# Performance work log

Hardware: AMD Instinct MI355X
Metric: run time of the kernel (lower is better)

## Reference

```python
import jax, jax.numpy as jnp
import numpy as np

N = 50000   # nodes
E = 600000  # directed edges (self-loops added inside reference, per GCNConv default)
G = 64      # graphs in the batch
D = 128     # in_features
H = 128     # hidden_channels
C = 10      # num_classes


def setup_inputs() -> dict:
    key = jax.random.key(0)
    ks = jax.random.split(key, 9)
    x = jax.random.normal(ks[0], (N, D), dtype=jnp.float32)
    edge_index = jax.random.randint(ks[1], (2, E), 0, N, dtype=jnp.int64)
    batch = jnp.sort(jax.random.randint(ks[2], (N,), 0, G, dtype=jnp.int64))
    # GCNConv weights (glorot-ish scale) and biases; final linear layer
    W1 = jax.random.normal(ks[3], (D, H), dtype=jnp.float32) / np.sqrt(D).astype(np.float32)
    b1 = jnp.zeros((H,), dtype=jnp.float32)
    W2 = jax.random.normal(ks[4], (H, H), dtype=jnp.float32) / np.sqrt(H).astype(np.float32)
    b2 = jnp.zeros((H,), dtype=jnp.float32)
    Wlin = jax.random.normal(ks[5], (H, C), dtype=jnp.float32) / np.sqrt(H).astype(np.float32)
    blin = jnp.zeros((C,), dtype=jnp.float32)
    return {"x": x, "W1": W1, "b1": b1, "W2": W2, "b2": b2,
            "Wlin": Wlin, "blin": blin, "edge_index": edge_index, "batch": batch}


def _gcn_conv(x, W, b, row, col, norm):
    # x' = D^{-1/2}(A+I)D^{-1/2} (x W) + b ; aggregate messages from row (src) into col (dst)
    h = x @ W                                   # [N, H] dense GEMM
    msg = norm[:, None] * h[row]                # gather by source index [E+N, H]
    out = jax.ops.segment_sum(msg, col, num_segments=N)  # scatter-add to targets
    return out + b


def reference(x, W1, b1, W2, b2, Wlin, blin, edge_index, batch):
    loops = jnp.arange(N, dtype=edge_index.dtype)
    row = jnp.concatenate([edge_index[0], loops])   # sources (+ self loops)
    col = jnp.concatenate([edge_index[1], loops])   # targets (+ self loops)
    # symmetric degree normalization (degrees >= 1 thanks to self loops)
    deg = jax.ops.segment_sum(jnp.ones_like(col, dtype=jnp.float32), col, num_segments=N)
    dinv = jax.lax.rsqrt(deg)
    norm = dinv[row] * dinv[col]                    # [E+N]

    h = jax.nn.relu(_gcn_conv(x, W1, b1, row, col, norm))
    h = _gcn_conv(h, W2, b2, row, col, norm)

    # global mean pool over graphs
    sums = jax.ops.segment_sum(h, batch, num_segments=G)                       # [G, H]
    cnt = jax.ops.segment_sum(jnp.ones((N,), dtype=jnp.float32), batch, num_segments=G)
    pooled = sums / jnp.maximum(cnt, 1.0)[:, None]

    return pooled @ Wlin + blin                     # logits [G, C]
```

## Files before the change

### kernel.cpp

```cpp
#include <hip/hip_runtime.h>

#define NN 50000
#define NE 600000
#define NG 64
#define DIM 128
#define NCLS 10
#define SB 196
#define NNP 50176
#define KBLK 392
#define KCH 128
#define CAP 64
#define E2B ((NE / 2 + 255) / 256)
#define NT32 (NNP / 32)
#define BSW_TAIL_START ((size_t)(NN >> 5) * 4096)

typedef unsigned short ushort;
typedef unsigned char uchar;
typedef __attribute__((ext_vector_type(8))) short short8;
typedef __attribute__((ext_vector_type(4))) float float4v;
typedef __attribute__((ext_vector_type(2))) float float2v;

__device__ __forceinline__ ushort f2bf(float f) {
    unsigned u = __float_as_uint(f);
    u += 0x7fff + ((u >> 16) & 1);
    return (ushort)(u >> 16);
}
__device__ __forceinline__ uchar f2fp8(float f) {
    int p = __builtin_amdgcn_cvt_pk_fp8_f32(f, f, 0, false);
    return (uchar)(p & 0xff);
}
__device__ __forceinline__ void accfp8(float* a, uint2 v) {
    float2v p0 = __builtin_amdgcn_cvt_pk_f32_fp8(v.x, false);
    float2v p1 = __builtin_amdgcn_cvt_pk_f32_fp8(v.x, true);
    float2v p2 = __builtin_amdgcn_cvt_pk_f32_fp8(v.y, false);
    float2v p3 = __builtin_amdgcn_cvt_pk_f32_fp8(v.y, true);
    a[0] += p0[0]; a[1] += p0[1]; a[2] += p1[0]; a[3] += p1[1];
    a[4] += p2[0]; a[5] += p2[1]; a[6] += p3[0]; a[7] += p3[1];
}

__global__ void k_init(int* __restrict__ cnt, const float* __restrict__ W1,
                       ushort* __restrict__ Wsw, float* __restrict__ T,
                       float* __restrict__ dinv, float* __restrict__ P,
                       ushort* __restrict__ Bsw) {
    int b = blockIdx.x, t = threadIdx.x;
    if (b < SB) {
        int i = b * 256 + t;
        if (i < NN) cnt[i] = 0;
    } else if (b < SB + 64) {
        int tid = (b - SB) * 256 + t;
        int j = tid & 7;
        int lane = (tid >> 3) & 63;
        int frag = tid >> 9;
        int nt = frag >> 2, kc = frag & 3;
        int k = kc * 32 + (lane >> 4) * 8 + j;
        int n = nt * 16 + (lane & 15);
        Wsw[tid] = f2bf(W1[k * DIM + n]);
    } else if (b < SB + 64 + 784) {
        float4* w4 = (float4*)T;
        int base = (b - SB - 64) * 256 + t;
#pragma unroll
        for (int i = 0; i < 4; ++i)
            w4[base + i * 200704] = make_float4(0.f, 0.f, 0.f, 0.f);
    } else if (b == SB + 64 + 784) {
        if (t < NNP - NN) dinv[NN + t] = 0.f;
        float4* p4 = (float4*)P;
#pragma unroll
        for (int i = 0; i < 8; ++i)
            p4[i * 256 + t] = make_float4(0.f, 0.f, 0.f, 0.f);
    } else {
        int idx = (b - (SB + 64 + 785)) * 256 + t;
        ((float4*)(Bsw + BSW_TAIL_START))[idx] = make_float4(0.f, 0.f, 0.f, 0.f);
    }
}

__global__ void k_fill(const int* __restrict__ row, const int* __restrict__ col,
                       int* __restrict__ cnt, int* __restrict__ ell) {
    int e = (blockIdx.x * blockDim.x + threadIdx.x) * 2;
    if (e < NE) {
        int2 r = *(const int2*)(row + e);
        int2 c = *(const int2*)(col + e);
        int p0 = atomicAdd(&cnt[c.x], 1);
        if (p0 < CAP) ell[c.x * CAP + p0] = r.x;
        int p1 = atomicAdd(&cnt[c.y], 1);
        if (p1 < CAP) ell[c.y * CAP + p1] = r.y;
    }
}

__global__ __launch_bounds__(256) void k_gemm_mfma(const float* __restrict__ Ain,
                                                   const ushort* __restrict__ Wsw,
                                                   const int* __restrict__ cnt,
                                                   uchar* __restrict__ Hs,
                                                   float* __restrict__ dinv) {
    const int t = threadIdx.x;
    const int wave = t >> 6, lane = t & 63;
    const int m = lane & 15, quad = lane >> 4;
    const int row0 = blockIdx.x * 64 + wave * 16;

    short8 bfrag[8][4];
#pragma unroll
    for (int nt = 0; nt < 8; ++nt)
#pragma unroll
        for (int kc = 0; kc < 4; ++kc)
            bfrag[nt][kc] = *(const short8*)(Wsw + ((nt * 4 + kc) * 64 + lane) * 8);

    float4v acc[8];
#pragma unroll
    for (int nt = 0; nt < 8; ++nt) acc[nt] = (float4v){0.f, 0.f, 0.f, 0.f};

    const int row = row0 + m;
    const int rclamp = row < NN ? row : NN - 1;

#pragma unroll
    for (int kc = 0; kc < 4; ++kc) {
        const float* ap = Ain + (size_t)rclamp * DIM + kc * 32 + quad * 8;
        float4 v0 = *(const float4*)ap;
        float4 v1 = *(const float4*)(ap + 4);
        union { short8 v; ushort u[8]; } tmp;
        tmp.u[0] = f2bf(v0.x); tmp.u[1] = f2bf(v0.y);
        tmp.u[2] = f2bf(v0.z); tmp.u[3] = f2bf(v0.w);
        tmp.u[4] = f2bf(v1.x); tmp.u[5] = f2bf(v1.y);
        tmp.u[6] = f2bf(v1.z); tmp.u[7] = f2bf(v1.w);
        short8 a = tmp.v;
#pragma unroll
        for (int nt = 0; nt < 8; ++nt)
            acc[nt] = __builtin_amdgcn_mfma_f32_16x16x32_bf16(a, bfrag[nt][kc], acc[nt], 0, 0, 0);
    }

#pragma unroll
    for (int reg = 0; reg < 4; ++reg) {
        int r = row0 + quad * 4 + reg;
        if (r < NN) {
            float d = rsqrtf(1.0f + (float)cnt[r]);
            if (m == 0) dinv[r] = d;
#pragma unroll
            for (int nt = 0; nt < 8; ++nt)
                Hs[(size_t)r * DIM + nt * 16 + m] = f2fp8(d * acc[nt][reg]);
        }
    }
}

__global__ __launch_bounds__(256) void k_gather_ell(const int* __restrict__ ell,
                                                    const int* __restrict__ deg,
                                                    const int* __restrict__ batch,
                                                    const float* __restrict__ bias,
                                                    const uchar* __restrict__ Hs,
                                                    float* __restrict__ T,
                                                    ushort* __restrict__ out) {
    int gt = blockIdx.x * blockDim.x + threadIdx.x;
    int node = gt >> 4, lane = gt & 15;
    if (node >= NN) return;
    const int* rowp = ell + node * CAP;
    int end = min(deg[node], CAP);
    const float d = rsqrtf(1.0f + (float)end);
    float* Trow = T + (size_t)batch[node] * NNP;
    const size_t off = (size_t)lane * 8;

    float a[8] = {0.f, 0.f, 0.f, 0.f, 0.f, 0.f, 0.f, 0.f};
    accfp8(a, *(const uint2*)(Hs + (size_t)node * DIM + off));
    if (lane == 0) atomicAdd(&Trow[node], d);

    int e = 0;
    for (; e + 8 <= end; e += 8) {
        int r0 = rowp[e], r1 = rowp[e + 1], r2 = rowp[e + 2], r3 = rowp[e + 3];
        int r4 = rowp[e + 4], r5 = rowp[e + 5], r6 = rowp[e + 6], r7 = rowp[e + 7];
        if (lane < 8) atomicAdd(&Trow[rowp[e + lane]], d);
        uint2 v0 = *(const uint2*)(Hs + (size_t)r0 * DIM + off);
        uint2 v1 = *(const uint2*)(Hs + (size_t)r1 * DIM + off);
        uint2 v2 = *(const uint2*)(Hs + (size_t)r2 * DIM + off);
        uint2 v3 = *(const uint2*)(Hs + (size_t)r3 * DIM + off);
        uint2 v4 = *(const uint2*)(Hs + (size_t)r4 * DIM + off);
        uint2 v5 = *(const uint2*)(Hs + (size_t)r5 * DIM + off);
        uint2 v6 = *(const uint2*)(Hs + (size_t)r6 * DIM + off);
        uint2 v7 = *(const uint2*)(Hs + (size_t)r7 * DIM + off);
        accfp8(a, v0); accfp8(a, v1); accfp8(a, v2); accfp8(a, v3);
        accfp8(a, v4); accfp8(a, v5); accfp8(a, v6); accfp8(a, v7);
    }
    for (; e + 4 <= end; e += 4) {
        int r0 = rowp[e], r1 = rowp[e + 1], r2 = rowp[e + 2], r3 = rowp[e + 3];
        if (lane < 4) atomicAdd(&Trow[rowp[e + lane]], d);
        uint2 v0 = *(const uint2*)(Hs + (size_t)r0 * DIM + off);
        uint2 v1 = *(const uint2*)(Hs + (size_t)r1 * DIM + off);
        uint2 v2 = *(const uint2*)(Hs + (size_t)r2 * DIM + off);
        uint2 v3 = *(const uint2*)(Hs + (size_t)r3 * DIM + off);
        accfp8(a, v0); accfp8(a, v1); accfp8(a, v2); accfp8(a, v3);
    }
    for (; e < end; ++e) {
        int r = rowp[e];
        if (lane == 0) atomicAdd(&Trow[r], d);
        accfp8(a, *(const uint2*)(Hs + (size_t)r * DIM + off));
    }

    float4 b0 = *(const float4*)(bias + off);
    float4 b1 = *(const float4*)(bias + off + 4);
    a[0] = fmaxf(fmaf(a[0], d, b0.x), 0.f); a[1] = fmaxf(fmaf(a[1], d, b0.y), 0.f);
    a[2] = fmaxf(fmaf(a[2], d, b0.z), 0.f); a[3] = fmaxf(fmaf(a[3], d, b0.w), 0.f);
    a[4] = fmaxf(fmaf(a[4], d, b1.x), 0.f); a[5] = fmaxf(fmaf(a[5], d, b1.y), 0.f);
    a[6] = fmaxf(fmaf(a[6], d, b1.z), 0.f); a[7] = fmaxf(fmaf(a[7], d, b1.w), 0.f);

    ushort* bp = out + (size_t)(node >> 5) * 4096 + (size_t)(lane >> 1) * 512
                     + (size_t)((node >> 3) & 3) * 128 + (size_t)(lane & 1) * 64
                     + (size_t)(node & 7);
    bp[0]  = f2bf(a[0]); bp[8]  = f2bf(a[1]); bp[16] = f2bf(a[2]); bp[24] = f2bf(a[3]);
    bp[32] = f2bf(a[4]); bp[40] = f2bf(a[5]); bp[48] = f2bf(a[6]); bp[56] = f2bf(a[7]);
}

__global__ __launch_bounds__(256) void k_pool_gemm(const float* __restrict__ T,
                                                   const float* __restrict__ dinv,
                                                   const ushort* __restrict__ Bsw,
                                                   float* __restrict__ P) {
    const int t = threadIdx.x;
    const int wave = t >> 6, lane = t & 63;
    const int m = lane & 15, quad = lane >> 4;
    const int g = wave * 16 + m;
    const int k0 = blockIdx.x * KCH;

    float4v acc[8];
#pragma unroll
    for (int nt = 0; nt < 8; ++nt) acc[nt] = (float4v){0.f, 0.f, 0.f, 0.f};

#pragma unroll
    for (int s = 0; s < KCH / 32; ++s) {
        const int kb = k0 + s * 32 + quad * 8;
        const float* ap = T + (size_t)g * NNP + kb;
        float4 a0 = *(const float4*)ap;
        float4 a1 = *(const float4*)(ap + 4);
        float4 d0 = *(const float4*)(dinv + kb);
        float4 d1 = *(const float4*)(dinv + kb + 4);
        union { short8 v; ushort u[8]; } af;
        af.u[0] = f2bf(a0.x * d0.x); af.u[1] = f2bf(a0.y * d0.y);
        af.u[2] = f2bf(a0.z * d0.z); af.u[3] = f2bf(a0.w * d0.w);
        af.u[4] = f2bf(a1.x * d1.x); af.u[5] = f2bf(a1.y * d1.y);
        af.u[6] = f2bf(a1.z * d1.z); af.u[7] = f2bf(a1.w * d1.w);

        const int t32 = (k0 >> 5) + s;
        const ushort* bb = Bsw + (size_t)t32 * 4096 + (size_t)lane * 8;
#pragma unroll
        for (int nt = 0; nt < 8; ++nt) {
            short8 bv = *(const short8*)(bb + nt * 512);
            acc[nt] = __builtin_amdgcn_mfma_f32_16x16x32_bf16(af.v, bv, acc[nt], 0, 0, 0);
        }
    }

#pragma unroll
    for (int reg = 0; reg < 4; ++reg) {
        int gg = wave * 16 + quad * 4 + reg;
#pragma unroll
        for (int nt = 0; nt < 8; ++nt)
            atomicAdd(&P[gg * DIM + nt * 16 + m], acc[nt][reg]);
    }
}

__global__ __launch_bounds__(128) void k_final(const float* __restrict__ P,
                                               const float* __restrict__ W2,
                                               const float* __restrict__ b2,
                                               const float* __restrict__ Wlin,
                                               const float* __restrict__ blin,
                                               const int* __restrict__ batch,
                                               float* __restrict__ out) {
    const int g = blockIdx.x;
    const int t = threadIdx.x;
    int start;
    { int a = 0, b = NN; while (a < b) { int m = (a + b) >> 1; if (batch[m] < g) a = m + 1; else b = m; } start = a; }
    int end;
    { int a = 0, b = NN; while (a < b) { int m = (a + b) >> 1; if (batch[m] < g + 1) a = m + 1; else b = m; } end = a; }
    const int cnt = end - start;

    __shared__ float Pl[DIM];
    Pl[t] = P[g * DIM + t];
    __syncthreads();
    float acc = 0.f;
    for (int k = 0; k < DIM; ++k) acc += Pl[k] * W2[k * DIM + t];
    __shared__ float pooled[DIM];
    pooled[t] = (cnt > 0) ? (acc / (float)cnt + b2[t]) : 0.f;
    __syncthreads();
    if (t < NCLS) {
        float s2 = blin[t];
        for (int k = 0; k < DIM; ++k) s2 += pooled[k] * Wlin[k * NCLS + t];
        out[g * NCLS + t] = s2;
    }
}

extern "C" void kernel_launch(void* const* d_in, const int* in_sizes, int n_in,
                              void* d_out, int out_size, void* d_ws, size_t ws_size,
                              hipStream_t stream) {
    const float* x    = (const float*)d_in[0];
    const float* W1   = (const float*)d_in[1];
    const float* b1   = (const float*)d_in[2];
    const float* W2   = (const float*)d_in[3];
    const float* b2   = (const float*)d_in[4];
    const float* Wlin = (const float*)d_in[5];
    const float* blin = (const float*)d_in[6];
    const int* eidx   = (const int*)d_in[7];
    const int* batch  = (const int*)d_in[8];
    float* out = (float*)d_out;

    char* ws = (char*)d_ws;
    int*    cnt   = (int*)(ws + 0);
    float*  dinv  = (float*)(ws + 200000);
    int*    ell   = (int*)(ws + 400704);
    ushort* Wsw   = (ushort*)(ws + 13200704);
    float*  T     = (float*)(ws + 13233472);
    uchar*  Hs1   = (uchar*)(ws + 26078528);
    ushort* Bsw   = (ushort*)(ws + 32478528);
    float*  P     = (float*)(ws + 45323584);

    const int* erow = eidx;
    const int* ecol = eidx + NE;

    k_init<<<SB + 64 + 784 + 1 + 12, 256, 0, stream>>>(cnt, W1, Wsw, T, dinv, P, Bsw);
    k_fill<<<E2B, 256, 0, stream>>>(erow, ecol, cnt, ell);

    const int gemm_grid = (NN + 63) / 64;
    const int node_grid = (NN * 16 + 255) / 256;

    k_gemm_mfma<<<gemm_grid, 256, 0, stream>>>(x, Wsw, cnt, Hs1, dinv);
    k_gather_ell<<<node_grid, 256, 0, stream>>>(ell, cnt, batch, b1, Hs1, T, Bsw);

    k_pool_gemm<<<KBLK, 256, 0, stream>>>(T, dinv, Bsw, P);

    k_final<<<NG, 128, 0, stream>>>(P, W2, b2, Wlin, blin, batch, out);
}
```

Before: 215.2 us.

## Compress ELL indices to u16, coalesce gather output via LDS, replace pool atomics with partials

Stores ELL neighbor indices as 16-bit values and loads them with vector loads, halving index traffic in fill and gather. The gather kernel now transposes its bf16 output through shared memory so the swizzled B-operand buffer is written in coalesced 16-byte stores instead of scattered 2-byte stores. The pooled GEMM writes per-block partial results instead of atomics, and the final kernel reduces the partials with 512 threads. The u16 indices rely on the node count fitting in 16 bits, and the extra barrier and partial buffer add some overhead.

```diff
diff --git a/kernel.cpp b/kernel.cpp
--- a/kernel.cpp
+++ b/kernel.cpp
@@ -11,7 +11,6 @@
 #define KCH 128
 #define CAP 64
 #define E2B ((NE / 2 + 255) / 256)
-#define NT32 (NNP / 32)
 #define BSW_TAIL_START ((size_t)(NN >> 5) * 4096)
 
 typedef unsigned short ushort;
@@ -40,8 +39,7 @@
 
 __global__ void k_init(int* __restrict__ cnt, const float* __restrict__ W1,
                        ushort* __restrict__ Wsw, float* __restrict__ T,
-                       float* __restrict__ dinv, float* __restrict__ P,
-                       ushort* __restrict__ Bsw) {
+                       float* __restrict__ dinv, ushort* __restrict__ Bsw) {
     int b = blockIdx.x, t = threadIdx.x;
     if (b < SB) {
         int i = b * 256 + t;
@@ -63,10 +61,6 @@
             w4[base + i * 200704] = make_float4(0.f, 0.f, 0.f, 0.f);
     } else if (b == SB + 64 + 784) {
         if (t < NNP - NN) dinv[NN + t] = 0.f;
-        float4* p4 = (float4*)P;
-#pragma unroll
-        for (int i = 0; i < 8; ++i)
-            p4[i * 256 + t] = make_float4(0.f, 0.f, 0.f, 0.f);
     } else {
         int idx = (b - (SB + 64 + 785)) * 256 + t;
         ((float4*)(Bsw + BSW_TAIL_START))[idx] = make_float4(0.f, 0.f, 0.f, 0.f);
@@ -74,15 +68,15 @@
 }
 
 __global__ void k_fill(const int* __restrict__ row, const int* __restrict__ col,
-                       int* __restrict__ cnt, int* __restrict__ ell) {
+                       int* __restrict__ cnt, ushort* __restrict__ ell) {
     int e = (blockIdx.x * blockDim.x + threadIdx.x) * 2;
     if (e < NE) {
         int2 r = *(const int2*)(row + e);
         int2 c = *(const int2*)(col + e);
         int p0 = atomicAdd(&cnt[c.x], 1);
-        if (p0 < CAP) ell[c.x * CAP + p0] = r.x;
+        if (p0 < CAP) ell[(size_t)c.x * CAP + p0] = (ushort)r.x;
         int p1 = atomicAdd(&cnt[c.y], 1);
-        if (p1 < CAP) ell[c.y * CAP + p1] = r.y;
+        if (p1 < CAP) ell[(size_t)c.y * CAP + p1] = (ushort)r.y;
     }
 }
 
@@ -139,17 +133,17 @@
     }
 }
 
-__global__ __launch_bounds__(256) void k_gather_ell(const int* __restrict__ ell,
+__global__ __launch_bounds__(256) void k_gather_ell(const ushort* __restrict__ ell,
                                                     const int* __restrict__ deg,
                                                     const int* __restrict__ batch,
                                                     const float* __restrict__ bias,
                                                     const uchar* __restrict__ Hs,
                                                     float* __restrict__ T,
-                                                    ushort* __restrict__ out) {
-    int gt = blockIdx.x * blockDim.x + threadIdx.x;
-    int node = gt >> 4, lane = gt & 15;
-    if (node >= NN) return;
-    const int* rowp = ell + node * CAP;
+                                                    ushort* __restrict__ Bsw) {
+    const int t = threadIdx.x, b = blockIdx.x;
+    const int tn = t >> 4, lane = t & 15;
+    const int node = b * 16 + tn;
+    const ushort* rowp = ell + (size_t)node * CAP;
     int end = min(deg[node], CAP);
     const float d = rsqrtf(1.0f + (float)end);
     float* Trow = T + (size_t)batch[node] * NNP;
@@ -161,8 +155,11 @@
 
     int e = 0;
     for (; e + 8 <= end; e += 8) {
-        int r0 = rowp[e], r1 = rowp[e + 1], r2 = rowp[e + 2], r3 = rowp[e + 3];
-        int r4 = rowp[e + 4], r5 = rowp[e + 5], r6 = rowp[e + 6], r7 = rowp[e + 7];
+        uint4 iv = *(const uint4*)(rowp + e);
+        int r0 = iv.x & 0xffff, r1 = iv.x >> 16;
+        int r2 = iv.y & 0xffff, r3 = iv.y >> 16;
+        int r4 = iv.z & 0xffff, r5 = iv.z >> 16;
+        int r6 = iv.w & 0xffff, r7 = iv.w >> 16;
         if (lane < 8) atomicAdd(&Trow[rowp[e + lane]], d);
         uint2 v0 = *(const uint2*)(Hs + (size_t)r0 * DIM + off);
         uint2 v1 = *(const uint2*)(Hs + (size_t)r1 * DIM + off);
@@ -176,7 +173,9 @@
         accfp8(a, v4); accfp8(a, v5); accfp8(a, v6); accfp8(a, v7);
     }
     for (; e + 4 <= end; e += 4) {
-        int r0 = rowp[e], r1 = rowp[e + 1], r2 = rowp[e + 2], r3 = rowp[e + 3];
+        uint2 lv = *(const uint2*)(rowp + e);
+        int r0 = lv.x & 0xffff, r1 = lv.x >> 16;
+        int r2 = lv.y & 0xffff, r3 = lv.y >> 16;
         if (lane < 4) atomicAdd(&Trow[rowp[e + lane]], d);
         uint2 v0 = *(const uint2*)(Hs + (size_t)r0 * DIM + off);
         uint2 v1 = *(const uint2*)(Hs + (size_t)r1 * DIM + off);
@@ -197,17 +196,31 @@
     a[4] = fmaxf(fmaf(a[4], d, b1.x), 0.f); a[5] = fmaxf(fmaf(a[5], d, b1.y), 0.f);
     a[6] = fmaxf(fmaf(a[6], d, b1.z), 0.f); a[7] = fmaxf(fmaf(a[7], d, b1.w), 0.f);
 
-    ushort* bp = out + (size_t)(node >> 5) * 4096 + (size_t)(lane >> 1) * 512
-                     + (size_t)((node >> 3) & 3) * 128 + (size_t)(lane & 1) * 64
-                     + (size_t)(node & 7);
-    bp[0]  = f2bf(a[0]); bp[8]  = f2bf(a[1]); bp[16] = f2bf(a[2]); bp[24] = f2bf(a[3]);
-    bp[32] = f2bf(a[4]); bp[40] = f2bf(a[5]); bp[48] = f2bf(a[6]); bp[56] = f2bf(a[7]);
+    __shared__ ushort Lb[16][128];
+    union { short8 v; ushort u[8]; } st;
+    st.u[0] = f2bf(a[0]); st.u[1] = f2bf(a[1]); st.u[2] = f2bf(a[2]); st.u[3] = f2bf(a[3]);
+    st.u[4] = f2bf(a[4]); st.u[5] = f2bf(a[5]); st.u[6] = f2bf(a[6]); st.u[7] = f2bf(a[7]);
+    *(short8*)(&Lb[tn][lane * 8]) = st.v;
+    __syncthreads();
+
+    const int nt = t >> 5, idx = t & 31;
+    const int a_rel = (idx >> 4) & 1, fb = (idx >> 3) & 1, f7 = idx & 7;
+    const int feat = nt * 16 + fb * 8 + f7;
+    const int nl = a_rel * 8;
+    uint4 o;
+    o.x = (unsigned)Lb[nl + 0][feat] | ((unsigned)Lb[nl + 1][feat] << 16);
+    o.y = (unsigned)Lb[nl + 2][feat] | ((unsigned)Lb[nl + 3][feat] << 16);
+    o.z = (unsigned)Lb[nl + 4][feat] | ((unsigned)Lb[nl + 5][feat] << 16);
+    o.w = (unsigned)Lb[nl + 6][feat] | ((unsigned)Lb[nl + 7][feat] << 16);
+    size_t base = (size_t)(b >> 1) * 4096 + (size_t)nt * 512
+                + (size_t)((b & 1) * 2 + a_rel) * 128 + (size_t)fb * 64 + (size_t)f7 * 8;
+    *(uint4*)(Bsw + base) = o;
 }
 
 __global__ __launch_bounds__(256) void k_pool_gemm(const float* __restrict__ T,
                                                    const float* __restrict__ dinv,
                                                    const ushort* __restrict__ Bsw,
-                                                   float* __restrict__ P) {
+                                                   float* __restrict__ partial) {
     const int t = threadIdx.x;
     const int wave = t >> 6, lane = t & 63;
     const int m = lane & 15, quad = lane >> 4;
@@ -241,16 +254,17 @@
         }
     }
 
+    float* dst = partial + (size_t)blockIdx.x * (NG * DIM);
 #pragma unroll
     for (int reg = 0; reg < 4; ++reg) {
         int gg = wave * 16 + quad * 4 + reg;
 #pragma unroll
         for (int nt = 0; nt < 8; ++nt)
-            atomicAdd(&P[gg * DIM + nt * 16 + m], acc[nt][reg]);
-    }
-}
-
-__global__ __launch_bounds__(128) void k_final(const float* __restrict__ P,
+            dst[gg * DIM + nt * 16 + m] = acc[nt][reg];
+    }
+}
+
+__global__ __launch_bounds__(512) void k_final(const float* __restrict__ partial,
                                                const float* __restrict__ W2,
                                                const float* __restrict__ b2,
                                                const float* __restrict__ Wlin,
@@ -259,19 +273,33 @@
                                                float* __restrict__ out) {
     const int g = blockIdx.x;
     const int t = threadIdx.x;
-    int start;
-    { int a = 0, b = NN; while (a < b) { int m = (a + b) >> 1; if (batch[m] < g) a = m + 1; else b = m; } start = a; }
-    int end;
-    { int a = 0, b = NN; while (a < b) { int m = (a + b) >> 1; if (batch[m] < g + 1) a = m + 1; else b = m; } end = a; }
-    const int cnt = end - start;
-
+    const int c = t & 127, h = t >> 7;
+
+    float s0 = 0.f, s1 = 0.f;
+    const float* pp = partial + (size_t)h * 98 * (NG * DIM) + g * DIM + c;
+#pragma unroll 7
+    for (int i = 0; i < 98; i += 2) {
+        s0 += pp[(size_t)i * (NG * DIM)];
+        s1 += pp[(size_t)(i + 1) * (NG * DIM)];
+    }
+
+    __shared__ float red[512];
     __shared__ float Pl[DIM];
-    Pl[t] = P[g * DIM + t];
+    __shared__ float pooled[DIM];
+    red[t] = s0 + s1;
     __syncthreads();
-    float acc = 0.f;
-    for (int k = 0; k < DIM; ++k) acc += Pl[k] * W2[k * DIM + t];
-    __shared__ float pooled[DIM];
-    pooled[t] = (cnt > 0) ? (acc / (float)cnt + b2[t]) : 0.f;
+    if (t < 128) Pl[t] = red[t] + red[t + 128] + red[t + 256] + red[t + 384];
+    __syncthreads();
+    if (t < 128) {
+        float acc = 0.f;
+        for (int k = 0; k < DIM; ++k) acc += Pl[k] * W2[k * DIM + t];
+        int start;
+        { int a = 0, bb = NN; while (a < bb) { int mm = (a + bb) >> 1; if (batch[mm] < g) a = mm + 1; else bb = mm; } start = a; }
+        int endp;
+        { int a = 0, bb = NN; while (a < bb) { int mm = (a + bb) >> 1; if (batch[mm] < g + 1) a = mm + 1; else bb = mm; } endp = a; }
+        const int cnt = endp - start;
+        pooled[t] = (cnt > 0) ? (acc / (float)cnt + b2[t]) : 0.f;
+    }
     __syncthreads();
     if (t < NCLS) {
         float s2 = blin[t];
@@ -297,26 +325,26 @@
     char* ws = (char*)d_ws;
     int*    cnt   = (int*)(ws + 0);
     float*  dinv  = (float*)(ws + 200000);
-    int*    ell   = (int*)(ws + 400704);
-    ushort* Wsw   = (ushort*)(ws + 13200704);
+    ushort* Wsw   = (ushort*)(ws + 400704);
+    ushort* ell   = (ushort*)(ws + 433472);
+    uchar*  Hs1   = (uchar*)(ws + 6833472);
     float*  T     = (float*)(ws + 13233472);
-    uchar*  Hs1   = (uchar*)(ws + 26078528);
-    ushort* Bsw   = (ushort*)(ws + 32478528);
-    float*  P     = (float*)(ws + 45323584);
+    ushort* Bsw   = (ushort*)(ws + 26078528);
+    float*  partial=(float*)(ws + 38923584);
 
     const int* erow = eidx;
     const int* ecol = eidx + NE;
 
-    k_init<<<SB + 64 + 784 + 1 + 12, 256, 0, stream>>>(cnt, W1, Wsw, T, dinv, P, Bsw);
+    k_init<<<SB + 64 + 784 + 1 + 12, 256, 0, stream>>>(cnt, W1, Wsw, T, dinv, Bsw);
     k_fill<<<E2B, 256, 0, stream>>>(erow, ecol, cnt, ell);
 
     const int gemm_grid = (NN + 63) / 64;
-    const int node_grid = (NN * 16 + 255) / 256;
+    const int node_grid = NN / 16;
 
     k_gemm_mfma<<<gemm_grid, 256, 0, stream>>>(x, Wsw, cnt, Hs1, dinv);
     k_gather_ell<<<node_grid, 256, 0, stream>>>(ell, cnt, batch, b1, Hs1, T, Bsw);
 
-    k_pool_gemm<<<KBLK, 256, 0, stream>>>(T, dinv, Bsw, P);
-
-    k_final<<<NG, 128, 0, stream>>>(P, W2, b2, Wlin, blin, batch, out);
-}
+    k_pool_gemm<<<KBLK, 256, 0, stream>>>(T, dinv, Bsw, partial);
+
+    k_final<<<NG, 512, 0, stream>>>(partial, W2, b2, Wlin, blin, batch, out);
+}
```

New measurement: 198.6 us. 1.08x faster.
